# Kernel tuning notes

Hardware: AMD Instinct MI355X
Metric: run time of the kernel (lower is better)

The kernel has to match this reference:

```python
import jax, jax.numpy as jnp
import numpy as np

B, S, D = 4, 2048, 512
H, DK, DV = 8, 64, 64
DFF = 2048
LN_EPS = 1e-5


def _layernorm(x, g, b):
    mu = jnp.mean(x, axis=-1, keepdims=True)
    var = jnp.mean(jnp.square(x - mu), axis=-1, keepdims=True)
    return (x - mu) * jax.lax.rsqrt(var + LN_EPS) * g + b


def setup_inputs() -> dict:
    key = jax.random.key(0)
    ks = jax.random.split(key, 9)
    def xavier(k, shape):
        fan_out, fan_in = shape
        std = np.sqrt(2.0 / (fan_in + fan_out))
        return jax.random.normal(k, shape, jnp.float32) * std
    GELU_GAIN = 1.85
    return {
        "x": jax.random.normal(ks[0], (B, S, D), jnp.float32),
        "attention_mask": jax.random.randint(ks[1], (B, S), 0, 2).astype(bool),
        "Wq": xavier(ks[2], (H * DK, D)),
        "Wk": xavier(ks[3], (H * DK, D)),
        "Wv": xavier(ks[4], (H * DV, D)),
        "Wp": xavier(ks[5], (D, H * DV)),
        "W1": xavier(ks[6], (DFF, D)) * GELU_GAIN,
        "b1": jnp.zeros((DFF,), jnp.float32),
        "W2": xavier(ks[7], (D, DFF)),
        "b2": jnp.zeros((D,), jnp.float32),
        "ln1_g": jnp.ones((D,), jnp.float32),
        "ln1_b": jnp.zeros((D,), jnp.float32),
        "ln2_g": jnp.ones((D,), jnp.float32),
        "ln2_b": jnp.zeros((D,), jnp.float32),
    }


def reference(x, attention_mask, Wq, Wk, Wv, Wp, W1, b1, W2, b2,
              ln1_g, ln1_b, ln2_g, ln2_b):
    b, s, d = x.shape
    residual = x
    q = (x @ Wq.T).reshape(b, s, H, DK)  # [B,S,H,DK]
    k = (x @ Wk.T).reshape(b, s, H, DK)
    v = (x @ Wv.T).reshape(b, s, H, DV)
    score = jnp.einsum("bshd,bthd->bhst", q, k) * (DK ** -0.5)  # [B,H,S,S]
    # subtractive mask: score -= 100 * not(mask)
    score = score - 100.0 * (~attention_mask)[:, None, None, :].astype(score.dtype)
    p = jax.nn.softmax(score, axis=-1)
    ctx = jnp.einsum("bhst,bthd->bshd", p, v).reshape(b, s, H * DV)
    att = ctx @ Wp.T  # dropout p=0.1 is identity in eval
    h = _layernorm(att + residual, ln1_g, ln1_b)
    ff = jax.nn.gelu(h @ W1.T + b1, approximate=False) @ W2.T + b2
    out = _layernorm(ff + h, ln2_g, ln2_b)
    return out
```

## Files before the change

kernel.cpp:

```cpp
#include <hip/hip_runtime.h>
#include <cstdint>
#include <cstddef>

#define B_ 4
#define S_ 2048
#define D_ 512
#define H_ 8
#define DK_ 64
#define DFF_ 2048

using s16x8  = __attribute__((ext_vector_type(8))) short;
using bf16x8 = __attribute__((ext_vector_type(8))) __bf16;
using f32x4  = __attribute__((ext_vector_type(4))) float;

__device__ __forceinline__ short f2bf(float f) {
  unsigned u = __builtin_bit_cast(unsigned, f);
  u += 0x7FFFu + ((u >> 16) & 1u);
  return (short)(u >> 16);
}
__device__ __forceinline__ float bf2f(short s) {
  unsigned u = ((unsigned)(unsigned short)s) << 16;
  return __builtin_bit_cast(float, u);
}

__device__ __forceinline__ void gl2lds16(const void* g, void* l) {
  __builtin_amdgcn_global_load_lds(
      (const __attribute__((address_space(1))) void*)g,
      (__attribute__((address_space(3))) void*)l, 16, 0, 0);
}

__global__ __launch_bounds__(256)
void cvt_all(const float* __restrict__ x, const float* __restrict__ Wq,
             const float* __restrict__ Wk, const float* __restrict__ Wv,
             const float* __restrict__ Wp, const float* __restrict__ W1,
             const float* __restrict__ W2,
             short* __restrict__ xb, short* __restrict__ wqkv,
             short* __restrict__ wp, short* __restrict__ w1, short* __restrict__ w2) {
  int blk = blockIdx.x;
  const float* src; short* dst; int off;
  if (blk < 4096)      { src = x;  dst = xb;            off = blk; }
  else if (blk < 4352) { src = Wq; dst = wqkv;          off = blk - 4096; }
  else if (blk < 4608) { src = Wk; dst = wqkv + 262144; off = blk - 4352; }
  else if (blk < 4864) { src = Wv; dst = wqkv + 524288; off = blk - 4608; }
  else if (blk < 5120) { src = Wp; dst = wp;            off = blk - 4864; }
  else if (blk < 6144) { src = W1; dst = w1;            off = blk - 5120; }
  else                 { src = W2; dst = w2;            off = blk - 6144; }
  int i = (off * 256 + threadIdx.x) * 4;
  float4 v = *(const float4*)(src + i);
  *(short4*)(dst + i) = make_short4(f2bf(v.x), f2bf(v.y), f2bf(v.z), f2bf(v.w));
}

template <int MODE>
__global__ __launch_bounds__(256)
void gemm_bt(const short* __restrict__ A, const short* __restrict__ B,
             int M, int N, int K,
             const float* __restrict__ aux1,
             void* __restrict__ out0, void* __restrict__ out1, void* __restrict__ out2) {
  __shared__ alignas(16) short As[128][64];
  __shared__ alignas(16) short Bs[128][64];

  const int tid  = threadIdx.x;
  const int lane = tid & 63;
  const int wave = tid >> 6;
  const int quad = lane >> 4;
  const int l16  = lane & 15;
  const int wm   = (wave >> 1) * 64;
  const int wn   = (wave & 1) * 64;
  const int bm   = blockIdx.x * 128;
  const int bn   = blockIdx.y * 128;
  const int Kh   = K / gridDim.z;
  const int koff = blockIdx.z * Kh;

  const int srow8 = lane >> 3;
  const int pb    = lane & 7;

  f32x4 acc[4][4] = {};

  for (int k0 = 0; k0 < Kh; k0 += 64) {
#pragma unroll
    for (int i = 0; i < 4; ++i) {
      const int rr = wave * 32 + i * 8 + srow8;
      const int cb = pb ^ (rr & 7);
      gl2lds16(A + (size_t)(bm + rr) * K + koff + k0 + cb * 8, &As[wave * 32 + i * 8][0]);
      gl2lds16(B + (size_t)(bn + rr) * K + koff + k0 + cb * 8, &Bs[wave * 32 + i * 8][0]);
    }
    __syncthreads();

#pragma unroll
    for (int c = 0; c < 2; ++c) {
      bf16x8 a[4], b[4];
#pragma unroll
      for (int i = 0; i < 4; ++i) {
        const int row = wm + i * 16 + l16;
        const int pba = (c * 4 + quad) ^ (row & 7);
        a[i] = __builtin_bit_cast(bf16x8, *(const s16x8*)&As[row][pba * 8]);
      }
#pragma unroll
      for (int j = 0; j < 4; ++j) {
        const int row = wn + j * 16 + l16;
        const int pbb = (c * 4 + quad) ^ (row & 7);
        b[j] = __builtin_bit_cast(bf16x8, *(const s16x8*)&Bs[row][pbb * 8]);
      }
#pragma unroll
      for (int i = 0; i < 4; ++i)
#pragma unroll
        for (int j = 0; j < 4; ++j)
          acc[i][j] = __builtin_amdgcn_mfma_f32_16x16x32_bf16(a[i], b[j], acc[i][j], 0, 0, 0);
    }
    __syncthreads();
  }

#pragma unroll
  for (int i = 0; i < 4; ++i) {
    const int m0 = bm + wm + i * 16 + quad * 4;
#pragma unroll
    for (int j = 0; j < 4; ++j) {
      const int n = bn + wn + j * 16 + l16;
      if constexpr (MODE == 0) {
        const int bb = m0 >> 11, ss0 = m0 & 2047;
        if (n < 512) {
          short4 pk = make_short4(f2bf(acc[i][j][0] * 0.125f), f2bf(acc[i][j][1] * 0.125f),
                                  f2bf(acc[i][j][2] * 0.125f), f2bf(acc[i][j][3] * 0.125f));
          *(short4*)((short*)out0 +
              ((((size_t)bb * H_ + (n >> 6)) * 64 + (n & 63)) * S_ + ss0)) = pk;
        } else if (n >= 1024) {
          const int nn = n - 1024;
          short4 pk = make_short4(f2bf(acc[i][j][0]), f2bf(acc[i][j][1]),
                                  f2bf(acc[i][j][2]), f2bf(acc[i][j][3]));
          *(short4*)((short*)out2 +
              ((((size_t)bb * H_ + (nn >> 6)) * 64 + (nn & 63)) * S_ + ss0)) = pk;
        } else {
          const int nn = n - 512;
          const size_t rowb = ((size_t)bb * H_ + (nn >> 6)) * S_ + ss0;
#pragma unroll
          for (int rr = 0; rr < 4; ++rr)
            ((short*)out1)[(rowb + rr) * 64 + (nn & 63)] = f2bf(acc[i][j][rr]);
        }
      } else if constexpr (MODE == 1) {
        float* dst = (float*)out0 + (size_t)blockIdx.z * M * N;
#pragma unroll
        for (int rr = 0; rr < 4; ++rr)
          dst[(size_t)(m0 + rr) * N + n] = acc[i][j][rr];
      } else {
#pragma unroll
        for (int rr = 0; rr < 4; ++rr) {
          float t = acc[i][j][rr] + aux1[n];
          float gl = 0.5f * t * (1.0f + erff(t * 0.70710678118f));
          ((short*)out0)[(size_t)(m0 + rr) * N + n] = f2bf(gl);
        }
      }
    }
  }
}

__global__ __launch_bounds__(256)
void flash_attn_mfma(const short* __restrict__ QTg, const short* __restrict__ Kb,
                     const short* __restrict__ Vtg, const void* __restrict__ mraw,
                     short* __restrict__ ctxb) {
  __shared__ alignas(16) short Ks[64][72];
  __shared__ alignas(16) short Vt[64][72];
  __shared__ alignas(16) short Ps[4][32][64];
  __shared__ alignas(16) float mrow[S_];
  __shared__ unsigned red[4];

  const int b = blockIdx.z, h = blockIdx.y;
  const int tid = threadIdx.x;
  const int w = tid >> 6, lane = tid & 63;
  const int quad = lane >> 4, l16 = lane & 15;
  const size_t base  = ((size_t)(b * H_ + h)) * S_ * DK_;
  const size_t baseT = ((size_t)(b * H_ + h)) * DK_ * S_;
  const int q0 = blockIdx.x * 128;

  {
    const unsigned* mw = (const unsigned*)mraw;
    unsigned v = 0;
#pragma unroll
    for (int i = 0; i < 8; ++i) v |= mw[tid + i * 256];
#pragma unroll
    for (int s = 1; s < 64; s <<= 1) v |= __shfl_xor(v, s);
    if (lane == 0) red[w] = v;
    __syncthreads();
    unsigned f = red[0] | red[1] | red[2] | red[3];
#pragma unroll
    for (int i = 0; i < 8; ++i) {
      int idx = tid + i * 256;
      int gidx = b * S_ + idx;
      int val;
      if ((f & ~1u) == 0u)            val = ((const int*)mraw)[gidx];
      else if (f == 0x3F800000u)      val = (((const float*)mraw)[gidx] != 0.0f);
      else                            val = ((const unsigned char*)mraw)[gidx];
      mrow[idx] = val ? 0.0f : -100.0f;
    }
  }

  bf16x8 qa[2][2];
#pragma unroll
  for (int st = 0; st < 2; ++st) {
    const int q = q0 + w * 32 + st * 16 + l16;
#pragma unroll
    for (int c = 0; c < 2; ++c) {
      s16x8 t;
#pragma unroll
      for (int j = 0; j < 8; ++j)
        t[j] = QTg[baseT + (size_t)(c * 32 + quad * 8 + j) * S_ + q];
      qa[st][c] = __builtin_bit_cast(bf16x8, t);
    }
  }

  f32x4 Oc[2][4] = {};
  float li[2][4] = {};
  const int swz = l16 & 7;

  const int r = tid >> 2, c16 = (tid & 3) * 16;
  const short* kp = Kb  + base  + (size_t)r * 64 + c16;
  const short* vp = Vtg + baseT + (size_t)r * S_ + c16;

  s16x8 kr0 = *(const s16x8*)(kp);
  s16x8 kr1 = *(const s16x8*)(kp + 8);
  s16x8 vr0 = *(const s16x8*)(vp);
  s16x8 vr1 = *(const s16x8*)(vp + 8);

  for (int t0 = 0; t0 < S_; t0 += 64) {
    __syncthreads();
    *(s16x8*)&Ks[r][c16]     = kr0;
    *(s16x8*)&Ks[r][c16 + 8] = kr1;
    *(s16x8*)&Vt[r][c16]     = vr0;
    *(s16x8*)&Vt[r][c16 + 8] = vr1;
    __syncthreads();

    if (t0 + 64 < S_) {
      kr0 = *(const s16x8*)(kp + (size_t)(t0 + 64) * 64);
      kr1 = *(const s16x8*)(kp + (size_t)(t0 + 64) * 64 + 8);
      vr0 = *(const s16x8*)(vp + t0 + 64);
      vr1 = *(const s16x8*)(vp + t0 + 64 + 8);
    }

    f32x4 sc[2][4] = {};
#pragma unroll
    for (int c = 0; c < 2; ++c) {
#pragma unroll
      for (int jt = 0; jt < 4; ++jt) {
        bf16x8 kb = __builtin_bit_cast(bf16x8,
            *(const s16x8*)&Ks[jt * 16 + l16][c * 32 + quad * 8]);
        sc[0][jt] = __builtin_amdgcn_mfma_f32_16x16x32_bf16(qa[0][c], kb, sc[0][jt], 0, 0, 0);
        sc[1][jt] = __builtin_amdgcn_mfma_f32_16x16x32_bf16(qa[1][c], kb, sc[1][jt], 0, 0, 0);
      }
    }

    float mb4[4];
#pragma unroll
    for (int jt = 0; jt < 4; ++jt) mb4[jt] = mrow[t0 + jt * 16 + l16];
#pragma unroll
    for (int st = 0; st < 2; ++st) {
#pragma unroll
      for (int jt = 0; jt < 4; ++jt) {
#pragma unroll
        for (int rr = 0; rr < 4; ++rr) {
          float p = __expf(sc[st][jt][rr] + mb4[jt]);
          unsigned u = __builtin_bit_cast(unsigned, p) & 0xFFFF0000u;
          li[st][rr] += __builtin_bit_cast(float, u);
          const int row = st * 16 + quad * 4 + rr;
          const int blk = (jt * 2 + (l16 >> 3)) ^ (row & 7);
          Ps[w][row][blk * 8 + (l16 & 7)] = (short)(u >> 16);
        }
      }
    }

#pragma unroll
    for (int c = 0; c < 2; ++c) {
      bf16x8 pa0 = __builtin_bit_cast(bf16x8,
          *(const s16x8*)&Ps[w][l16][((c * 4 + quad) ^ swz) * 8]);
      bf16x8 pa1 = __builtin_bit_cast(bf16x8,
          *(const s16x8*)&Ps[w][16 + l16][((c * 4 + quad) ^ swz) * 8]);
#pragma unroll
      for (int dt = 0; dt < 4; ++dt) {
        bf16x8 vb = __builtin_bit_cast(bf16x8,
            *(const s16x8*)&Vt[dt * 16 + l16][c * 32 + quad * 8]);
        Oc[0][dt] = __builtin_amdgcn_mfma_f32_16x16x32_bf16(pa0, vb, Oc[0][dt], 0, 0, 0);
        Oc[1][dt] = __builtin_amdgcn_mfma_f32_16x16x32_bf16(pa1, vb, Oc[1][dt], 0, 0, 0);
      }
    }
  }

#pragma unroll
  for (int st = 0; st < 2; ++st) {
#pragma unroll
    for (int rr = 0; rr < 4; ++rr) {
      float l = li[st][rr];
#pragma unroll
      for (int m = 1; m < 16; m <<= 1) l += __shfl_xor(l, m);
      float inv = 1.f / l;
      const size_t row = (size_t)b * S_ + q0 + w * 32 + st * 16 + quad * 4 + rr;
#pragma unroll
      for (int dt = 0; dt < 4; ++dt)
        ctxb[row * (H_ * DK_) + h * 64 + dt * 16 + l16] = f2bf(Oc[st][dt][rr] * inv);
    }
  }
}

__global__ __launch_bounds__(256)
void ln_fused(const float* __restrict__ p0, const float* __restrict__ p1,
              const float* __restrict__ xres, const short* __restrict__ hres,
              const float* __restrict__ bias,
              const float* __restrict__ g, const float* __restrict__ bb,
              float* __restrict__ out32, short* __restrict__ outb) {
  const int wave = threadIdx.x >> 6, lane = threadIdx.x & 63;
  const int token = blockIdx.x * 4 + wave;
  const size_t off = (size_t)token * D_;
  const int c = lane * 8;

  float v[8];
  {
    float4 a0 = *(const float4*)(p0 + off + c);
    float4 a1 = *(const float4*)(p0 + off + c + 4);
    float4 b0 = *(const float4*)(p1 + off + c);
    float4 b1 = *(const float4*)(p1 + off + c + 4);
    v[0]=a0.x+b0.x; v[1]=a0.y+b0.y; v[2]=a0.z+b0.z; v[3]=a0.w+b0.w;
    v[4]=a1.x+b1.x; v[5]=a1.y+b1.y; v[6]=a1.z+b1.z; v[7]=a1.w+b1.w;
  }
  if (xres) {
    float4 x0 = *(const float4*)(xres + off + c);
    float4 x1 = *(const float4*)(xres + off + c + 4);
    v[0]+=x0.x; v[1]+=x0.y; v[2]+=x0.z; v[3]+=x0.w;
    v[4]+=x1.x; v[5]+=x1.y; v[6]+=x1.z; v[7]+=x1.w;
  }
  if (hres) {
    short4 h0 = *(const short4*)(hres + off + c);
    short4 h1 = *(const short4*)(hres + off + c + 4);
    v[0]+=bf2f(h0.x); v[1]+=bf2f(h0.y); v[2]+=bf2f(h0.z); v[3]+=bf2f(h0.w);
    v[4]+=bf2f(h1.x); v[5]+=bf2f(h1.y); v[6]+=bf2f(h1.z); v[7]+=bf2f(h1.w);
  }
  if (bias) {
    float4 c0 = *(const float4*)(bias + c);
    float4 c1 = *(const float4*)(bias + c + 4);
    v[0]+=c0.x; v[1]+=c0.y; v[2]+=c0.z; v[3]+=c0.w;
    v[4]+=c1.x; v[5]+=c1.y; v[6]+=c1.z; v[7]+=c1.w;
  }

  float sum = 0.f;
#pragma unroll
  for (int i = 0; i < 8; ++i) sum += v[i];
#pragma unroll
  for (int m = 1; m < 64; m <<= 1) sum += __shfl_xor(sum, m);
  float mu = sum * (1.0f / D_);
  float vs = 0.f;
#pragma unroll
  for (int i = 0; i < 8; ++i) { v[i] -= mu; vs += v[i] * v[i]; }
#pragma unroll
  for (int m = 1; m < 64; m <<= 1) vs += __shfl_xor(vs, m);
  float rstd = rsqrtf(vs * (1.0f / D_) + 1e-5f);
#pragma unroll
  for (int i = 0; i < 8; ++i) {
    float val = v[i] * rstd * g[c + i] + bb[c + i];
    if (out32) out32[off + c + i] = val;
    if (outb)  outb[off + c + i] = f2bf(val);
  }
}

constexpr size_t OFF_XB   = 0;
constexpr size_t OFF_WQKV = 8388608;
constexpr size_t OFF_WP   = 9961472;
constexpr size_t OFF_W1   = 10485760;
constexpr size_t OFF_W2   = 12582912;
constexpr size_t OFF_QT   = 14680064;
constexpr size_t OFF_K    = 23068672;
constexpr size_t OFF_VT   = 31457280;
constexpr size_t OFF_CTX  = 39845888;
constexpr size_t OFF_P0   = 48234496;
constexpr size_t OFF_P1   = 65011712;
constexpr size_t OFF_HB   = 81788928;
constexpr size_t OFF_FF1  = 14680064;
constexpr size_t WS_NEED  = 90177536;

extern "C" void kernel_launch(void* const* d_in, const int* in_sizes, int n_in,
                              void* d_out, int out_size, void* d_ws, size_t ws_size,
                              hipStream_t stream) {
  if (ws_size < WS_NEED) return;

  const float* x    = (const float*)d_in[0];
  const void*  msk  = d_in[1];
  const float* Wq   = (const float*)d_in[2];
  const float* Wk   = (const float*)d_in[3];
  const float* Wv   = (const float*)d_in[4];
  const float* Wp   = (const float*)d_in[5];
  const float* W1   = (const float*)d_in[6];
  const float* b1   = (const float*)d_in[7];
  const float* W2   = (const float*)d_in[8];
  const float* b2   = (const float*)d_in[9];
  const float* ln1g = (const float*)d_in[10];
  const float* ln1b = (const float*)d_in[11];
  const float* ln2g = (const float*)d_in[12];
  const float* ln2b = (const float*)d_in[13];

  char* ws = (char*)d_ws;
  short* xb    = (short*)(ws + OFF_XB);
  short* wqkv  = (short*)(ws + OFF_WQKV);
  short* Wpb   = (short*)(ws + OFF_WP);
  short* W1b   = (short*)(ws + OFF_W1);
  short* W2b   = (short*)(ws + OFF_W2);
  short* QTb   = (short*)(ws + OFF_QT);
  short* Kbh   = (short*)(ws + OFF_K);
  short* VTb   = (short*)(ws + OFF_VT);
  short* ctxb  = (short*)(ws + OFF_CTX);
  float* p0    = (float*)(ws + OFF_P0);
  short* hb    = (short*)(ws + OFF_HB);
  short* ff1b  = (short*)(ws + OFF_FF1);

  cvt_all<<<7168, 256, 0, stream>>>(x, Wq, Wk, Wv, Wp, W1, W2,
                                    xb, wqkv, Wpb, W1b, W2b);

  gemm_bt<0><<<dim3(64, 12, 1), 256, 0, stream>>>(xb, wqkv, 8192, 1536, 512,
                                                  nullptr, QTb, Kbh, VTb);

  flash_attn_mfma<<<dim3(S_ / 128, H_, B_), 256, 0, stream>>>(QTb, Kbh, VTb, msk, ctxb);

  gemm_bt<1><<<dim3(64, 4, 2), 256, 0, stream>>>(ctxb, Wpb, 8192, 512, 512,
                                                 nullptr, p0, nullptr, nullptr);

  ln_fused<<<2048, 256, 0, stream>>>(p0, p0 + (size_t)8192 * 512, x, nullptr, nullptr,
                                     ln1g, ln1b, nullptr, hb);

  gemm_bt<2><<<dim3(64, 16, 1), 256, 0, stream>>>(hb, W1b, 8192, 2048, 512,
                                                  b1, ff1b, nullptr, nullptr);

  gemm_bt<1><<<dim3(64, 4, 2), 256, 0, stream>>>(ff1b, W2b, 8192, 512, 2048,
                                                 nullptr, p0, nullptr, nullptr);

  ln_fused<<<2048, 256, 0, stream>>>(p0, p0 + (size_t)8192 * 512, nullptr, hb, b2,
                                     ln2g, ln2b, (float*)d_out, nullptr);
}
```

Baseline: 314.9 us.

## Split attention block into 8 waves of 16 query rows with MFMA priority hints

The flash attention kernel now runs 512 threads per block, and each of the 8 waves handles 16 query rows instead of 32. Per-thread K/V staging loads are halved and register pressure per wave drops. s_setprio brackets around the MFMA sections favour matrix issue over the softmax work. The trade-off is that each K/V tile loaded into LDS is reused over fewer rows per wave, and LDS reads per MFMA go up.

```diff
diff --git a/kernel.cpp b/kernel.cpp
--- a/kernel.cpp
+++ b/kernel.cpp
@@ -153,15 +153,15 @@
   }
 }
 
-__global__ __launch_bounds__(256)
+__global__ __launch_bounds__(512)
 void flash_attn_mfma(const short* __restrict__ QTg, const short* __restrict__ Kb,
                      const short* __restrict__ Vtg, const void* __restrict__ mraw,
                      short* __restrict__ ctxb) {
   __shared__ alignas(16) short Ks[64][72];
   __shared__ alignas(16) short Vt[64][72];
-  __shared__ alignas(16) short Ps[4][32][64];
+  __shared__ alignas(16) short Ps[8][16][64];
   __shared__ alignas(16) float mrow[S_];
-  __shared__ unsigned red[4];
+  __shared__ unsigned red[8];
 
   const int b = blockIdx.z, h = blockIdx.y;
   const int tid = threadIdx.x;
@@ -175,15 +175,16 @@
     const unsigned* mw = (const unsigned*)mraw;
     unsigned v = 0;
 #pragma unroll
-    for (int i = 0; i < 8; ++i) v |= mw[tid + i * 256];
+    for (int i = 0; i < 4; ++i) v |= mw[tid + i * 512];
 #pragma unroll
     for (int s = 1; s < 64; s <<= 1) v |= __shfl_xor(v, s);
     if (lane == 0) red[w] = v;
     __syncthreads();
-    unsigned f = red[0] | red[1] | red[2] | red[3];
-#pragma unroll
-    for (int i = 0; i < 8; ++i) {
-      int idx = tid + i * 256;
+    unsigned f = red[0] | red[1] | red[2] | red[3] |
+                 red[4] | red[5] | red[6] | red[7];
+#pragma unroll
+    for (int i = 0; i < 4; ++i) {
+      int idx = tid + i * 512;
       int gidx = b * S_ + idx;
       int val;
       if ((f & ~1u) == 0u)            val = ((const int*)mraw)[gidx];
@@ -193,108 +194,95 @@
     }
   }
 
-  bf16x8 qa[2][2];
-#pragma unroll
-  for (int st = 0; st < 2; ++st) {
-    const int q = q0 + w * 32 + st * 16 + l16;
+  bf16x8 qa[2];
+  {
+    const int q = q0 + w * 16 + l16;
 #pragma unroll
     for (int c = 0; c < 2; ++c) {
       s16x8 t;
 #pragma unroll
       for (int j = 0; j < 8; ++j)
         t[j] = QTg[baseT + (size_t)(c * 32 + quad * 8 + j) * S_ + q];
-      qa[st][c] = __builtin_bit_cast(bf16x8, t);
-    }
-  }
-
-  f32x4 Oc[2][4] = {};
-  float li[2][4] = {};
+      qa[c] = __builtin_bit_cast(bf16x8, t);
+    }
+  }
+
+  f32x4 Oc[4] = {};
+  float li[4] = {};
   const int swz = l16 & 7;
 
-  const int r = tid >> 2, c16 = (tid & 3) * 16;
-  const short* kp = Kb  + base  + (size_t)r * 64 + c16;
-  const short* vp = Vtg + baseT + (size_t)r * S_ + c16;
-
-  s16x8 kr0 = *(const s16x8*)(kp);
-  s16x8 kr1 = *(const s16x8*)(kp + 8);
-  s16x8 vr0 = *(const s16x8*)(vp);
-  s16x8 vr1 = *(const s16x8*)(vp + 8);
+  const int r = tid >> 3, c8 = (tid & 7) * 8;
+  const short* kp = Kb  + base  + (size_t)r * 64 + c8;
+  const short* vp = Vtg + baseT + (size_t)r * S_ + c8;
+
+  s16x8 kr = *(const s16x8*)(kp);
+  s16x8 vr = *(const s16x8*)(vp);
 
   for (int t0 = 0; t0 < S_; t0 += 64) {
     __syncthreads();
-    *(s16x8*)&Ks[r][c16]     = kr0;
-    *(s16x8*)&Ks[r][c16 + 8] = kr1;
-    *(s16x8*)&Vt[r][c16]     = vr0;
-    *(s16x8*)&Vt[r][c16 + 8] = vr1;
+    *(s16x8*)&Ks[r][c8] = kr;
+    *(s16x8*)&Vt[r][c8] = vr;
     __syncthreads();
 
     if (t0 + 64 < S_) {
-      kr0 = *(const s16x8*)(kp + (size_t)(t0 + 64) * 64);
-      kr1 = *(const s16x8*)(kp + (size_t)(t0 + 64) * 64 + 8);
-      vr0 = *(const s16x8*)(vp + t0 + 64);
-      vr1 = *(const s16x8*)(vp + t0 + 64 + 8);
-    }
-
-    f32x4 sc[2][4] = {};
+      kr = *(const s16x8*)(kp + (size_t)(t0 + 64) * 64);
+      vr = *(const s16x8*)(vp + (t0 + 64));
+    }
+
+    f32x4 sc[4] = {};
+    __builtin_amdgcn_s_setprio(1);
 #pragma unroll
     for (int c = 0; c < 2; ++c) {
 #pragma unroll
       for (int jt = 0; jt < 4; ++jt) {
         bf16x8 kb = __builtin_bit_cast(bf16x8,
             *(const s16x8*)&Ks[jt * 16 + l16][c * 32 + quad * 8]);
-        sc[0][jt] = __builtin_amdgcn_mfma_f32_16x16x32_bf16(qa[0][c], kb, sc[0][jt], 0, 0, 0);
-        sc[1][jt] = __builtin_amdgcn_mfma_f32_16x16x32_bf16(qa[1][c], kb, sc[1][jt], 0, 0, 0);
-      }
-    }
+        sc[jt] = __builtin_amdgcn_mfma_f32_16x16x32_bf16(qa[c], kb, sc[jt], 0, 0, 0);
+      }
+    }
+    __builtin_amdgcn_s_setprio(0);
 
     float mb4[4];
 #pragma unroll
     for (int jt = 0; jt < 4; ++jt) mb4[jt] = mrow[t0 + jt * 16 + l16];
 #pragma unroll
-    for (int st = 0; st < 2; ++st) {
-#pragma unroll
-      for (int jt = 0; jt < 4; ++jt) {
-#pragma unroll
-        for (int rr = 0; rr < 4; ++rr) {
-          float p = __expf(sc[st][jt][rr] + mb4[jt]);
-          unsigned u = __builtin_bit_cast(unsigned, p) & 0xFFFF0000u;
-          li[st][rr] += __builtin_bit_cast(float, u);
-          const int row = st * 16 + quad * 4 + rr;
-          const int blk = (jt * 2 + (l16 >> 3)) ^ (row & 7);
-          Ps[w][row][blk * 8 + (l16 & 7)] = (short)(u >> 16);
-        }
-      }
-    }
-
+    for (int jt = 0; jt < 4; ++jt) {
+#pragma unroll
+      for (int rr = 0; rr < 4; ++rr) {
+        float p = __expf(sc[jt][rr] + mb4[jt]);
+        unsigned u = __builtin_bit_cast(unsigned, p) & 0xFFFF0000u;
+        li[rr] += __builtin_bit_cast(float, u);
+        const int row = quad * 4 + rr;
+        const int blk = (jt * 2 + (l16 >> 3)) ^ (row & 7);
+        Ps[w][row][blk * 8 + (l16 & 7)] = (short)(u >> 16);
+      }
+    }
+
+    __builtin_amdgcn_s_setprio(1);
 #pragma unroll
     for (int c = 0; c < 2; ++c) {
-      bf16x8 pa0 = __builtin_bit_cast(bf16x8,
+      bf16x8 pa = __builtin_bit_cast(bf16x8,
           *(const s16x8*)&Ps[w][l16][((c * 4 + quad) ^ swz) * 8]);
-      bf16x8 pa1 = __builtin_bit_cast(bf16x8,
-          *(const s16x8*)&Ps[w][16 + l16][((c * 4 + quad) ^ swz) * 8]);
 #pragma unroll
       for (int dt = 0; dt < 4; ++dt) {
         bf16x8 vb = __builtin_bit_cast(bf16x8,
             *(const s16x8*)&Vt[dt * 16 + l16][c * 32 + quad * 8]);
-        Oc[0][dt] = __builtin_amdgcn_mfma_f32_16x16x32_bf16(pa0, vb, Oc[0][dt], 0, 0, 0);
-        Oc[1][dt] = __builtin_amdgcn_mfma_f32_16x16x32_bf16(pa1, vb, Oc[1][dt], 0, 0, 0);
-      }
-    }
-  }
-
-#pragma unroll
-  for (int st = 0; st < 2; ++st) {
-#pragma unroll
-    for (int rr = 0; rr < 4; ++rr) {
-      float l = li[st][rr];
-#pragma unroll
-      for (int m = 1; m < 16; m <<= 1) l += __shfl_xor(l, m);
-      float inv = 1.f / l;
-      const size_t row = (size_t)b * S_ + q0 + w * 32 + st * 16 + quad * 4 + rr;
-#pragma unroll
-      for (int dt = 0; dt < 4; ++dt)
-        ctxb[row * (H_ * DK_) + h * 64 + dt * 16 + l16] = f2bf(Oc[st][dt][rr] * inv);
-    }
+        Oc[dt] = __builtin_amdgcn_mfma_f32_16x16x32_bf16(pa, vb, Oc[dt], 0, 0, 0);
+      }
+    }
+    __builtin_amdgcn_s_setprio(0);
+  }
+
+#pragma unroll
+  for (int rr = 0; rr < 4; ++rr) {
+    float l = li[rr];
+#pragma unroll
+    for (int m = 1; m < 16; m <<= 1) l += __shfl_xor(l, m);
+    float inv = 1.f / l;
+    const size_t row = (size_t)b * S_ + q0 + w * 16 + quad * 4 + rr;
+#pragma unroll
+    for (int dt = 0; dt < 4; ++dt)
+      ctxb[row * (H_ * DK_) + h * 64 + dt * 16 + l16] = f2bf(Oc[dt][rr] * inv);
   }
 }
 
@@ -412,7 +400,7 @@
   gemm_bt<0><<<dim3(64, 12, 1), 256, 0, stream>>>(xb, wqkv, 8192, 1536, 512,
                                                   nullptr, QTb, Kbh, VTb);
 
-  flash_attn_mfma<<<dim3(S_ / 128, H_, B_), 256, 0, stream>>>(QTb, Kbh, VTb, msk, ctxb);
+  flash_attn_mfma<<<dim3(S_ / 128, H_, B_), 512, 0, stream>>>(QTb, Kbh, VTb, msk, ctxb);
 
   gemm_bt<1><<<dim3(64, 4, 2), 256, 0, stream>>>(ctxb, Wpb, 8192, 512, 512,
                                                  nullptr, p0, nullptr, nullptr);
```

Result: slower. 322.6 us (+2.5%).

## Transpose score MFMA, swizzle K/V LDS tiles, and pack attention mask into bits

Applied to the files above, without the earlier changes.

Swaps the MFMA operand order so each lane holds scores for one query row across four keys. That allows vectorized uint2 writes of P into LDS and a single per-lane row-sum accumulator. K and V tiles drop their padding and use an XOR swizzle to avoid bank conflicts. The mask is stored as a bit array in LDS and applied by zeroing p instead of adding -100, and s_setprio raises priority around the MFMA sections. This relies on masked scores being negligible (exp(-100) treated as zero) and on the transposed accumulator layout being indexed correctly.

```diff
diff --git a/kernel.cpp b/kernel.cpp
--- a/kernel.cpp
+++ b/kernel.cpp
@@ -157,10 +157,10 @@
 void flash_attn_mfma(const short* __restrict__ QTg, const short* __restrict__ Kb,
                      const short* __restrict__ Vtg, const void* __restrict__ mraw,
                      short* __restrict__ ctxb) {
-  __shared__ alignas(16) short Ks[64][72];
-  __shared__ alignas(16) short Vt[64][72];
+  __shared__ alignas(16) short Ks[64][64];
+  __shared__ alignas(16) short Vt[64][64];
   __shared__ alignas(16) short Ps[4][32][64];
-  __shared__ alignas(16) float mrow[S_];
+  __shared__ alignas(8) unsigned char mbits8[256];
   __shared__ unsigned red[4];
 
   const int b = blockIdx.z, h = blockIdx.y;
@@ -181,16 +181,18 @@
     if (lane == 0) red[w] = v;
     __syncthreads();
     unsigned f = red[0] | red[1] | red[2] | red[3];
-#pragma unroll
-    for (int i = 0; i < 8; ++i) {
-      int idx = tid + i * 256;
-      int gidx = b * S_ + idx;
+    unsigned byte = 0;
+#pragma unroll
+    for (int j = 0; j < 8; ++j) {
+      int t = tid * 8 + j;
+      int gidx = b * S_ + t;
       int val;
       if ((f & ~1u) == 0u)            val = ((const int*)mraw)[gidx];
       else if (f == 0x3F800000u)      val = (((const float*)mraw)[gidx] != 0.0f);
       else                            val = ((const unsigned char*)mraw)[gidx];
-      mrow[idx] = val ? 0.0f : -100.0f;
-    }
+      byte |= (val ? 1u : 0u) << j;
+    }
+    mbits8[tid] = (unsigned char)byte;
   }
 
   bf16x8 qa[2][2];
@@ -208,12 +210,14 @@
   }
 
   f32x4 Oc[2][4] = {};
-  float li[2][4] = {};
+  float li[2] = {};
   const int swz = l16 & 7;
 
-  const int r = tid >> 2, c16 = (tid & 3) * 16;
-  const short* kp = Kb  + base  + (size_t)r * 64 + c16;
-  const short* vp = Vtg + baseT + (size_t)r * S_ + c16;
+  const int r = tid >> 2, cc = tid & 3;
+  const short* kp = Kb  + base  + (size_t)r * 64 + cc * 16;
+  const short* vp = Vtg + baseT + (size_t)r * S_ + cc * 16;
+  const int ch0 = (((cc * 2)     ^ (r & 7)) << 3);
+  const int ch1 = (((cc * 2 + 1) ^ (r & 7)) << 3);
 
   s16x8 kr0 = *(const s16x8*)(kp);
   s16x8 kr1 = *(const s16x8*)(kp + 8);
@@ -222,74 +226,83 @@
 
   for (int t0 = 0; t0 < S_; t0 += 64) {
     __syncthreads();
-    *(s16x8*)&Ks[r][c16]     = kr0;
-    *(s16x8*)&Ks[r][c16 + 8] = kr1;
-    *(s16x8*)&Vt[r][c16]     = vr0;
-    *(s16x8*)&Vt[r][c16 + 8] = vr1;
+    *(s16x8*)&Ks[r][ch0] = kr0;
+    *(s16x8*)&Ks[r][ch1] = kr1;
+    *(s16x8*)&Vt[r][ch0] = vr0;
+    *(s16x8*)&Vt[r][ch1] = vr1;
     __syncthreads();
 
     if (t0 + 64 < S_) {
       kr0 = *(const s16x8*)(kp + (size_t)(t0 + 64) * 64);
       kr1 = *(const s16x8*)(kp + (size_t)(t0 + 64) * 64 + 8);
-      vr0 = *(const s16x8*)(vp + t0 + 64);
-      vr1 = *(const s16x8*)(vp + t0 + 64 + 8);
+      vr0 = *(const s16x8*)(vp + (t0 + 64));
+      vr1 = *(const s16x8*)(vp + (t0 + 64) + 8);
     }
 
     f32x4 sc[2][4] = {};
+    __builtin_amdgcn_s_setprio(1);
 #pragma unroll
     for (int c = 0; c < 2; ++c) {
 #pragma unroll
       for (int jt = 0; jt < 4; ++jt) {
         bf16x8 kb = __builtin_bit_cast(bf16x8,
-            *(const s16x8*)&Ks[jt * 16 + l16][c * 32 + quad * 8]);
-        sc[0][jt] = __builtin_amdgcn_mfma_f32_16x16x32_bf16(qa[0][c], kb, sc[0][jt], 0, 0, 0);
-        sc[1][jt] = __builtin_amdgcn_mfma_f32_16x16x32_bf16(qa[1][c], kb, sc[1][jt], 0, 0, 0);
-      }
-    }
-
-    float mb4[4];
-#pragma unroll
-    for (int jt = 0; jt < 4; ++jt) mb4[jt] = mrow[t0 + jt * 16 + l16];
-#pragma unroll
-    for (int st = 0; st < 2; ++st) {
-#pragma unroll
-      for (int jt = 0; jt < 4; ++jt) {
+            *(const s16x8*)&Ks[jt * 16 + l16][((c * 4 + quad) ^ swz) << 3]);
+        sc[0][jt] = __builtin_amdgcn_mfma_f32_16x16x32_bf16(kb, qa[0][c], sc[0][jt], 0, 0, 0);
+        sc[1][jt] = __builtin_amdgcn_mfma_f32_16x16x32_bf16(kb, qa[1][c], sc[1][jt], 0, 0, 0);
+      }
+    }
+    __builtin_amdgcn_s_setprio(0);
+
+    const unsigned long long mball =
+        *(const unsigned long long*)&mbits8[t0 >> 3];
+#pragma unroll
+    for (int jt = 0; jt < 4; ++jt) {
+      const unsigned m16 = ((unsigned)(mball >> (jt * 16))) >> (quad * 4);
+      const int pch = (((jt * 2 + (quad >> 1)) ^ swz) << 3) + (quad & 1) * 4;
+#pragma unroll
+      for (int st = 0; st < 2; ++st) {
+        unsigned uu[4];
 #pragma unroll
         for (int rr = 0; rr < 4; ++rr) {
-          float p = __expf(sc[st][jt][rr] + mb4[jt]);
-          unsigned u = __builtin_bit_cast(unsigned, p) & 0xFFFF0000u;
-          li[st][rr] += __builtin_bit_cast(float, u);
-          const int row = st * 16 + quad * 4 + rr;
-          const int blk = (jt * 2 + (l16 >> 3)) ^ (row & 7);
-          Ps[w][row][blk * 8 + (l16 & 7)] = (short)(u >> 16);
+          float pe = __expf(sc[st][jt][rr]);
+          unsigned u = __builtin_bit_cast(unsigned, pe) & 0xFFFF0000u;
+          u = ((m16 >> rr) & 1u) ? u : 0u;
+          li[st] += __builtin_bit_cast(float, u);
+          uu[rr] = u;
         }
-      }
-    }
-
+        *(uint2*)&Ps[w][st * 16 + l16][pch] =
+            make_uint2((uu[0] >> 16) | (uu[1] & 0xFFFF0000u),
+                       (uu[2] >> 16) | (uu[3] & 0xFFFF0000u));
+      }
+    }
+
+    __builtin_amdgcn_s_setprio(1);
 #pragma unroll
     for (int c = 0; c < 2; ++c) {
       bf16x8 pa0 = __builtin_bit_cast(bf16x8,
-          *(const s16x8*)&Ps[w][l16][((c * 4 + quad) ^ swz) * 8]);
+          *(const s16x8*)&Ps[w][l16][((c * 4 + quad) ^ swz) << 3]);
       bf16x8 pa1 = __builtin_bit_cast(bf16x8,
-          *(const s16x8*)&Ps[w][16 + l16][((c * 4 + quad) ^ swz) * 8]);
+          *(const s16x8*)&Ps[w][16 + l16][((c * 4 + quad) ^ swz) << 3]);
 #pragma unroll
       for (int dt = 0; dt < 4; ++dt) {
         bf16x8 vb = __builtin_bit_cast(bf16x8,
-            *(const s16x8*)&Vt[dt * 16 + l16][c * 32 + quad * 8]);
+            *(const s16x8*)&Vt[dt * 16 + l16][((c * 4 + quad) ^ swz) << 3]);
         Oc[0][dt] = __builtin_amdgcn_mfma_f32_16x16x32_bf16(pa0, vb, Oc[0][dt], 0, 0, 0);
         Oc[1][dt] = __builtin_amdgcn_mfma_f32_16x16x32_bf16(pa1, vb, Oc[1][dt], 0, 0, 0);
       }
     }
+    __builtin_amdgcn_s_setprio(0);
   }
 
 #pragma unroll
   for (int st = 0; st < 2; ++st) {
+    float l = li[st];
+    l += __shfl_xor(l, 16);
+    l += __shfl_xor(l, 32);
 #pragma unroll
     for (int rr = 0; rr < 4; ++rr) {
-      float l = li[st][rr];
-#pragma unroll
-      for (int m = 1; m < 16; m <<= 1) l += __shfl_xor(l, m);
-      float inv = 1.f / l;
+      float lr = __shfl(l, quad * 4 + rr);
+      float inv = 1.f / lr;
       const size_t row = (size_t)b * S_ + q0 + w * 32 + st * 16 + quad * 4 + rr;
 #pragma unroll
       for (int dt = 0; dt < 4; ++dt)
```

Result: no change. 310.2 us (-1.5%).
